# Optimization experiments

Hardware: AMD Instinct MI355X
Metric: run time of the kernel (lower is better)

## Reference

```python
import jax, jax.numpy as jnp
import numpy as np

N_NODES = 50000
N_EDGES = 800000
C = 16          # in = hidden = out channels
FE = 8          # num_edge_features
NUM_GRAPHS = 64


def _nnconv(x, src, dst, edge_attr, w_e, b_e, root, bias):
    # edge MLP -> per-edge weight matrix [E, Cin, Cout]
    cin = x.shape[1]
    W = (edge_attr @ w_e + b_e).reshape(-1, cin, root.shape[1])
    msg = jnp.einsum('ei,eio->eo', x[src], W)            # gather + per-edge matvec
    n = x.shape[0]
    agg = jax.ops.segment_sum(msg, dst, num_segments=n)  # scatter-add
    cnt = jax.ops.segment_sum(jnp.ones((msg.shape[0], 1), x.dtype), dst, num_segments=n)
    agg = agg / jnp.maximum(cnt, 1.0)                    # aggr='mean'
    return x @ root + agg + bias


def setup_inputs() -> dict:
    key = jax.random.key(0)
    ks = jax.random.split(key, 12)
    x = jax.random.normal(ks[0], (N_NODES, C), dtype=jnp.float32)
    edge_index = jax.random.randint(ks[1], (2, N_EDGES), 0, N_NODES, dtype=jnp.int64)
    edge_attr = jax.random.uniform(ks[2], (N_EDGES, FE), dtype=jnp.float32)
    batch = jnp.sort(jax.random.randint(ks[3], (N_NODES,), 0, NUM_GRAPHS, dtype=jnp.int64))
    s = 1.0 / np.sqrt(C)
    se = 1.0 / np.sqrt(FE)
    we1 = jax.random.normal(ks[4], (FE, C * C), dtype=jnp.float32) * se
    be1 = jnp.zeros((C * C,), dtype=jnp.float32)
    root1 = jax.random.normal(ks[5], (C, C), dtype=jnp.float32) * s
    bias1 = jnp.zeros((C,), dtype=jnp.float32)
    we2 = jax.random.normal(ks[6], (FE, C * C), dtype=jnp.float32) * se
    be2 = jnp.zeros((C * C,), dtype=jnp.float32)
    root2 = jax.random.normal(ks[7], (C, C), dtype=jnp.float32) * s
    bias2 = jnp.zeros((C,), dtype=jnp.float32)
    return {"x": x, "edge_index": edge_index, "edge_attr": edge_attr, "batch": batch,
            "we1": we1, "be1": be1, "root1": root1, "bias1": bias1,
            "we2": we2, "be2": be2, "root2": root2, "bias2": bias2}


def reference(x, edge_index, edge_attr, batch,
              we1, be1, root1, bias1, we2, be2, root2, bias2):
    src, dst = edge_index[0], edge_index[1]
    # layer 1 (activation=None -> identity; dropout_prob=0 -> identity)
    h = _nnconv(x, src, dst, edge_attr, we1, be1, root1, bias1)
    # layer 2
    h = _nnconv(h, src, dst, edge_attr, we2, be2, root2, bias2)
    # global mean pool per graph, then flatten
    sums = jax.ops.segment_sum(h, batch, num_segments=NUM_GRAPHS)
    cnts = jax.ops.segment_sum(jnp.ones((h.shape[0], 1), h.dtype), batch, num_segments=NUM_GRAPHS)
    pooled = sums / jnp.maximum(cnts, 1.0)
    return pooled.reshape(-1)
```

## Files before the change

kernel.cpp:

```cpp
#include <hip/hip_runtime.h>

#define NN 50000
#define NE 800000
#define NG 64
#define NB ((NN + 255) / 256)
#define WSTR 164

__global__ __launch_bounds__(256) void histk(const int* __restrict__ dst,
                                             int* __restrict__ deg) {
    int e = blockIdx.x * 256 + threadIdx.x;
    if (e < NE) atomicAdd(&deg[dst[e]], 1);
}

__global__ __launch_bounds__(256) void bsumk(const int* __restrict__ deg,
                                             int* __restrict__ bsum) {
    int idx = blockIdx.x * 256 + threadIdx.x;
    int v = (idx < NN) ? deg[idx] : 0;
#pragma unroll
    for (int off = 32; off > 0; off >>= 1) v += __shfl_down(v, off);
    __shared__ int ws[4];
    int lane = threadIdx.x & 63, w = threadIdx.x >> 6;
    if (lane == 0) ws[w] = v;
    __syncthreads();
    if (threadIdx.x == 0) bsum[blockIdx.x] = ws[0] + ws[1] + ws[2] + ws[3];
}

__global__ __launch_bounds__(256) void bscank(const int* __restrict__ bsum,
                                              int* __restrict__ boffs) {
    int tid = threadIdx.x;
    int v = (tid < NB) ? bsum[tid] : 0;
    int lane = tid & 63, w = tid >> 6;
    int t = v;
#pragma unroll
    for (int off = 1; off < 64; off <<= 1) {
        int u = __shfl_up(t, off);
        if (lane >= off) t += u;
    }
    __shared__ int ws[4];
    if (lane == 63) ws[w] = t;
    __syncthreads();
    int add = 0;
    for (int k = 0; k < w; k++) add += ws[k];
    if (tid < NB) boffs[tid] = add + t - v;
}

__global__ __launch_bounds__(256) void fscank(const int* __restrict__ deg,
                                              const int* __restrict__ boffs,
                                              int* __restrict__ row,
                                              int* __restrict__ cur) {
    int idx = blockIdx.x * 256 + threadIdx.x;
    int v = (idx < NN) ? deg[idx] : 0;
    int lane = threadIdx.x & 63, w = threadIdx.x >> 6;
    int t = v;
#pragma unroll
    for (int off = 1; off < 64; off <<= 1) {
        int u = __shfl_up(t, off);
        if (lane >= off) t += u;
    }
    __shared__ int ws[4];
    if (lane == 63) ws[w] = t;
    __syncthreads();
    int add = boffs[blockIdx.x];
    for (int k = 0; k < w; k++) add += ws[k];
    int ex = add + t - v;
    if (idx < NN) { row[idx] = ex; cur[idx] = ex; }
    else if (idx == NN) row[NN] = ex;
}

__global__ __launch_bounds__(256) void scatk(const int* __restrict__ src,
                                             const int* __restrict__ dst,
                                             const float* __restrict__ ea,
                                             int* __restrict__ cur,
                                             float* __restrict__ rec) {
    int e = blockIdx.x * 256 + threadIdx.x;
    if (e >= NE) return;
    int d = dst[e];
    int pos = atomicAdd(&cur[d], 1);
    float4 a = *(const float4*)(ea + (size_t)e * 8);
    float4 b = *(const float4*)(ea + (size_t)e * 8 + 4);
    float4* r = (float4*)(rec + (size_t)pos * 16);
    float4 r0; r0.x = __int_as_float(src[e]); r0.y = a.x; r0.z = a.y; r0.w = a.z;
    float4 r1; r1.x = a.w; r1.y = b.x; r1.z = b.y; r1.w = b.z;
    float4 r2; r2.x = b.w; r2.y = 0.f; r2.z = 0.f; r2.w = 0.f;
    float4 r3; r3.x = 0.f; r3.y = 0.f; r3.z = 0.f; r3.w = 0.f;
    r[0] = r0; r[1] = r1; r[2] = r2; r[3] = r3;
}

template <bool POOL>
__global__ __launch_bounds__(256) void fusedk(const float* __restrict__ xin,
                                              const int* __restrict__ row,
                                              const float* __restrict__ rec,
                                              const float* __restrict__ we,
                                              const float* __restrict__ be,
                                              const float* __restrict__ root,
                                              const float* __restrict__ bias,
                                              const int* __restrict__ batch,
                                              float* __restrict__ out,
                                              float* __restrict__ gsum,
                                              float* __restrict__ gcnt) {
    __shared__ float wt[16 * WSTR];
    __shared__ float pls[16][WSTR];
    __shared__ float bs[16];
    __shared__ float gacc[16][16];
    __shared__ int gcnta[16];
    int tid = threadIdx.x;
    for (int idx = tid; idx < 2048; idx += 256) {
        int f = idx >> 8; int i = (idx >> 4) & 15; int o = idx & 15;
        wt[o * WSTR + f * 16 + i] = we[idx];
    }
    {
        int i = tid >> 4, o = tid & 15;
        wt[o * WSTR + 128 + i] = be[tid];
        wt[o * WSTR + 144 + i] = root[tid];
    }
    if (tid < 16) bs[tid] = bias[tid];
    if (POOL) {
        gacc[tid >> 4][tid & 15] = 0.f;
        if (tid < 16) gcnta[tid] = 0;
    }

    int g = tid >> 4, t = tid & 15;
    int v = blockIdx.x * 16 + g;
    int r0 = row[v], r1 = row[v + 1];

    float p0 = 0.f, p1 = 0.f, p2 = 0.f, p3 = 0.f;
    float p4 = 0.f, p5 = 0.f, p6 = 0.f, p7 = 0.f, s = 0.f;
    for (int pos = r0; pos < r1; ++pos) {
        const float4* rp = (const float4*)(rec + (size_t)pos * 16);
        float4 c0 = rp[0];
        float4 c1 = rp[1];
        float4 c2 = rp[2];
        int sn = __float_as_int(c0.x);
        float xv = xin[(size_t)sn * 16 + t];
        p0 += c0.y * xv; p1 += c0.z * xv; p2 += c0.w * xv; p3 += c1.x * xv;
        p4 += c1.y * xv; p5 += c1.z * xv; p6 += c1.w * xv; p7 += c2.x * xv;
        s += xv;
    }
    pls[g][0 * 16 + t] = p0; pls[g][1 * 16 + t] = p1;
    pls[g][2 * 16 + t] = p2; pls[g][3 * 16 + t] = p3;
    pls[g][4 * 16 + t] = p4; pls[g][5 * 16 + t] = p5;
    pls[g][6 * 16 + t] = p6; pls[g][7 * 16 + t] = p7;
    pls[g][128 + t] = s;
    pls[g][144 + t] = xin[(size_t)v * 16 + t];
    __syncthreads();

    int o = t;
    const float4* pv = (const float4*)pls[g];
    const float4* wc = (const float4*)(wt + o * WSTR);
    float agg = 0.f;
#pragma unroll
    for (int k = 0; k < 36; k++) {
        float4 a = pv[k]; float4 wv = wc[k];
        agg += a.x * wv.x + a.y * wv.y + a.z * wv.z + a.w * wv.w;
    }
    float r = 0.f;
#pragma unroll
    for (int k = 36; k < 40; k++) {
        float4 a = pv[k]; float4 wv = wc[k];
        r += a.x * wv.x + a.y * wv.y + a.z * wv.z + a.w * wv.w;
    }
    int dg = r1 - r0;
    float h = r + agg / (float)(dg > 1 ? dg : 1) + bs[o];

    if (!POOL) {
        out[(size_t)v * 16 + o] = h;
    } else {
        int bmin = batch[blockIdx.x * 16];
        int b = batch[v];
        int slot = b - bmin;
        if (slot < 16) {
            atomicAdd(&gacc[slot][o], h);
            if (o == 0) atomicAdd(&gcnta[slot], 1);
        } else {
            atomicAdd(&gsum[(size_t)b * 16 + o], h);
            if (o == 0) atomicAdd(&gcnt[b], 1.0f);
        }
        __syncthreads();
        if (gcnta[g] > 0) {
            atomicAdd(&gsum[(size_t)(bmin + g) * 16 + o], gacc[g][o]);
            if (o == 0) atomicAdd(&gcnt[bmin + g], (float)gcnta[g]);
        }
    }
}

__global__ void fink(const float* __restrict__ gsum,
                     const float* __restrict__ gcnt,
                     float* __restrict__ out) {
    int i = blockIdx.x * 256 + threadIdx.x;
    if (i < NG * 16) out[i] = gsum[i] / fmaxf(gcnt[i >> 4], 1.0f);
}

extern "C" void kernel_launch(void* const* d_in, const int* in_sizes, int n_in,
                              void* d_out, int out_size, void* d_ws, size_t ws_size,
                              hipStream_t stream) {
    const float* x     = (const float*)d_in[0];
    const int*   ei    = (const int*)d_in[1];
    const float* ea    = (const float*)d_in[2];
    const int*   batch = (const int*)d_in[3];
    const float* we1   = (const float*)d_in[4];
    const float* be1   = (const float*)d_in[5];
    const float* root1 = (const float*)d_in[6];
    const float* bias1 = (const float*)d_in[7];
    const float* we2   = (const float*)d_in[8];
    const float* be2   = (const float*)d_in[9];
    const float* root2 = (const float*)d_in[10];
    const float* bias2 = (const float*)d_in[11];

    float* ws = (float*)d_ws;
    float* rec  = ws;
    float* h1   = rec + (size_t)NE * 16;
    int*   row  = (int*)(h1 + (size_t)NN * 16);
    int*   cur  = row + NN + 1;
    int*   deg  = cur + NN;
    int*   bsum = deg + NN;
    int*   boffs= bsum + NB;
    float* gsum = (float*)(boffs + NB);
    float* gcnt = gsum + NG * 16;

    hipMemsetAsync(deg, 0, (size_t)(NN + 2 * NB + NG * 16 + NG) * 4, stream);

    const int* src = ei;
    const int* dst = ei + NE;

    int gE = (NE + 255) / 256;
    int gV = NN / 16;

    histk<<<gE, 256, 0, stream>>>(dst, deg);
    bsumk<<<NB, 256, 0, stream>>>(deg, bsum);
    bscank<<<1, 256, 0, stream>>>(bsum, boffs);
    fscank<<<NB, 256, 0, stream>>>(deg, boffs, row, cur);
    scatk<<<gE, 256, 0, stream>>>(src, dst, ea, cur, rec);

    fusedk<false><<<gV, 256, 0, stream>>>(x, row, rec, we1, be1, root1, bias1,
                                          batch, h1, gsum, gcnt);
    fusedk<true><<<gV, 256, 0, stream>>>(h1, row, rec, we2, be2, root2, bias2,
                                         batch, h1 , gsum, gcnt);

    fink<<<4, 256, 0, stream>>>(gsum, gcnt, (float*)d_out);
}
```

Measured before the change: 206.2 us.

## Split edge records into compact attr and src arrays, batch gathers in fused kernel

The per-edge CSR record shrinks from 64 bytes (src plus padded attributes) to 32 bytes of attributes, with source indices moved to a separate int array. The scatter kernel writes both with nontemporal stores. The fused aggregation loop loads 16 source indices cooperatively and broadcasts them with shuffles, and it unrolls the x gathers four at a time to raise memory-level parallelism. The aim is to halve record traffic in both layers and hide gather latency, at the cost of larger code and remainder loops.

```diff
diff --git a/kernel.cpp b/kernel.cpp
--- a/kernel.cpp
+++ b/kernel.cpp
@@ -5,6 +5,8 @@
 #define NG 64
 #define NB ((NN + 255) / 256)
 #define WSTR 164
+
+typedef float nfloat4 __attribute__((ext_vector_type(4)));
 
 __global__ __launch_bounds__(256) void histk(const int* __restrict__ dst,
                                              int* __restrict__ deg) {
@@ -71,25 +73,25 @@
                                              const int* __restrict__ dst,
                                              const float* __restrict__ ea,
                                              int* __restrict__ cur,
-                                             float* __restrict__ rec) {
+                                             float* __restrict__ rec,
+                                             int* __restrict__ srcp) {
     int e = blockIdx.x * 256 + threadIdx.x;
     if (e >= NE) return;
     int d = dst[e];
     int pos = atomicAdd(&cur[d], 1);
-    float4 a = *(const float4*)(ea + (size_t)e * 8);
-    float4 b = *(const float4*)(ea + (size_t)e * 8 + 4);
-    float4* r = (float4*)(rec + (size_t)pos * 16);
-    float4 r0; r0.x = __int_as_float(src[e]); r0.y = a.x; r0.z = a.y; r0.w = a.z;
-    float4 r1; r1.x = a.w; r1.y = b.x; r1.z = b.y; r1.w = b.z;
-    float4 r2; r2.x = b.w; r2.y = 0.f; r2.z = 0.f; r2.w = 0.f;
-    float4 r3; r3.x = 0.f; r3.y = 0.f; r3.z = 0.f; r3.w = 0.f;
-    r[0] = r0; r[1] = r1; r[2] = r2; r[3] = r3;
+    nfloat4 a = *(const nfloat4*)(ea + (size_t)e * 8);
+    nfloat4 b = *(const nfloat4*)(ea + (size_t)e * 8 + 4);
+    nfloat4* r = (nfloat4*)(rec + (size_t)pos * 8);
+    __builtin_nontemporal_store(a, r);
+    __builtin_nontemporal_store(b, r + 1);
+    __builtin_nontemporal_store(src[e], &srcp[pos]);
 }
 
 template <bool POOL>
 __global__ __launch_bounds__(256) void fusedk(const float* __restrict__ xin,
                                               const int* __restrict__ row,
                                               const float* __restrict__ rec,
+                                              const int* __restrict__ srcp,
                                               const float* __restrict__ we,
                                               const float* __restrict__ be,
                                               const float* __restrict__ root,
@@ -120,22 +122,76 @@
     }
 
     int g = tid >> 4, t = tid & 15;
+    int wl = tid & 63;
+    int gl = wl & ~15;
     int v = blockIdx.x * 16 + g;
     int r0 = row[v], r1 = row[v + 1];
 
     float p0 = 0.f, p1 = 0.f, p2 = 0.f, p3 = 0.f;
     float p4 = 0.f, p5 = 0.f, p6 = 0.f, p7 = 0.f, s = 0.f;
-    for (int pos = r0; pos < r1; ++pos) {
-        const float4* rp = (const float4*)(rec + (size_t)pos * 16);
-        float4 c0 = rp[0];
-        float4 c1 = rp[1];
-        float4 c2 = rp[2];
-        int sn = __float_as_int(c0.x);
+
+    int full_end = r0 + ((r1 - r0) & ~15);
+    for (int base = r0; base < full_end; base += 16) {
+        int sv = srcp[base + t];
+#pragma unroll
+        for (int c = 0; c < 16; c += 4) {
+            int s0 = __shfl(sv, gl + c + 0);
+            int s1 = __shfl(sv, gl + c + 1);
+            int s2 = __shfl(sv, gl + c + 2);
+            int s3 = __shfl(sv, gl + c + 3);
+            float x0 = xin[(size_t)s0 * 16 + t];
+            float x1 = xin[(size_t)s1 * 16 + t];
+            float x2 = xin[(size_t)s2 * 16 + t];
+            float x3 = xin[(size_t)s3 * 16 + t];
+            const float4* q0 = (const float4*)(rec + (size_t)(base + c) * 8);
+            float4 a0 = q0[0], b0 = q0[1];
+            float4 a1 = q0[2], b1 = q0[3];
+            float4 a2 = q0[4], b2 = q0[5];
+            float4 a3 = q0[6], b3 = q0[7];
+            p0 += a0.x * x0; p1 += a0.y * x0; p2 += a0.z * x0; p3 += a0.w * x0;
+            p4 += b0.x * x0; p5 += b0.y * x0; p6 += b0.z * x0; p7 += b0.w * x0; s += x0;
+            p0 += a1.x * x1; p1 += a1.y * x1; p2 += a1.z * x1; p3 += a1.w * x1;
+            p4 += b1.x * x1; p5 += b1.y * x1; p6 += b1.z * x1; p7 += b1.w * x1; s += x1;
+            p0 += a2.x * x2; p1 += a2.y * x2; p2 += a2.z * x2; p3 += a2.w * x2;
+            p4 += b2.x * x2; p5 += b2.y * x2; p6 += b2.z * x2; p7 += b2.w * x2; s += x2;
+            p0 += a3.x * x3; p1 += a3.y * x3; p2 += a3.z * x3; p3 += a3.w * x3;
+            p4 += b3.x * x3; p5 += b3.y * x3; p6 += b3.z * x3; p7 += b3.w * x3; s += x3;
+        }
+    }
+    int pos = full_end;
+    int pend = full_end + ((r1 - full_end) & ~3);
+    for (; pos < pend; pos += 4) {
+        int s0 = srcp[pos + 0];
+        int s1 = srcp[pos + 1];
+        int s2 = srcp[pos + 2];
+        int s3 = srcp[pos + 3];
+        float x0 = xin[(size_t)s0 * 16 + t];
+        float x1 = xin[(size_t)s1 * 16 + t];
+        float x2 = xin[(size_t)s2 * 16 + t];
+        float x3 = xin[(size_t)s3 * 16 + t];
+        const float4* q = (const float4*)(rec + (size_t)pos * 8);
+        float4 a0 = q[0], b0 = q[1];
+        float4 a1 = q[2], b1 = q[3];
+        float4 a2 = q[4], b2 = q[5];
+        float4 a3 = q[6], b3 = q[7];
+        p0 += a0.x * x0; p1 += a0.y * x0; p2 += a0.z * x0; p3 += a0.w * x0;
+        p4 += b0.x * x0; p5 += b0.y * x0; p6 += b0.z * x0; p7 += b0.w * x0; s += x0;
+        p0 += a1.x * x1; p1 += a1.y * x1; p2 += a1.z * x1; p3 += a1.w * x1;
+        p4 += b1.x * x1; p5 += b1.y * x1; p6 += b1.z * x1; p7 += b1.w * x1; s += x1;
+        p0 += a2.x * x2; p1 += a2.y * x2; p2 += a2.z * x2; p3 += a2.w * x2;
+        p4 += b2.x * x2; p5 += b2.y * x2; p6 += b2.z * x2; p7 += b2.w * x2; s += x2;
+        p0 += a3.x * x3; p1 += a3.y * x3; p2 += a3.z * x3; p3 += a3.w * x3;
+        p4 += b3.x * x3; p5 += b3.y * x3; p6 += b3.z * x3; p7 += b3.w * x3; s += x3;
+    }
+    for (; pos < r1; ++pos) {
+        int sn = srcp[pos];
         float xv = xin[(size_t)sn * 16 + t];
-        p0 += c0.y * xv; p1 += c0.z * xv; p2 += c0.w * xv; p3 += c1.x * xv;
-        p4 += c1.y * xv; p5 += c1.z * xv; p6 += c1.w * xv; p7 += c2.x * xv;
-        s += xv;
-    }
+        const float4* q = (const float4*)(rec + (size_t)pos * 8);
+        float4 a = q[0], b = q[1];
+        p0 += a.x * xv; p1 += a.y * xv; p2 += a.z * xv; p3 += a.w * xv;
+        p4 += b.x * xv; p5 += b.y * xv; p6 += b.z * xv; p7 += b.w * xv; s += xv;
+    }
+
     pls[g][0 * 16 + t] = p0; pls[g][1 * 16 + t] = p1;
     pls[g][2 * 16 + t] = p2; pls[g][3 * 16 + t] = p3;
     pls[g][4 * 16 + t] = p4; pls[g][5 * 16 + t] = p5;
@@ -208,8 +264,9 @@
 
     float* ws = (float*)d_ws;
     float* rec  = ws;
-    float* h1   = rec + (size_t)NE * 16;
-    int*   row  = (int*)(h1 + (size_t)NN * 16);
+    float* h1   = rec + (size_t)NE * 8;
+    int*   srcp = (int*)(h1 + (size_t)NN * 16);
+    int*   row  = srcp + NE;
     int*   cur  = row + NN + 1;
     int*   deg  = cur + NN;
     int*   bsum = deg + NN;
@@ -229,11 +286,11 @@
     bsumk<<<NB, 256, 0, stream>>>(deg, bsum);
     bscank<<<1, 256, 0, stream>>>(bsum, boffs);
     fscank<<<NB, 256, 0, stream>>>(deg, boffs, row, cur);
-    scatk<<<gE, 256, 0, stream>>>(src, dst, ea, cur, rec);
-
-    fusedk<false><<<gV, 256, 0, stream>>>(x, row, rec, we1, be1, root1, bias1,
+    scatk<<<gE, 256, 0, stream>>>(src, dst, ea, cur, rec, srcp);
+
+    fusedk<false><<<gV, 256, 0, stream>>>(x, row, rec, srcp, we1, be1, root1, bias1,
                                           batch, h1, gsum, gcnt);
-    fusedk<true><<<gV, 256, 0, stream>>>(h1, row, rec, we2, be2, root2, bias2,
+    fusedk<true><<<gV, 256, 0, stream>>>(h1, row, rec, srcp, we2, be2, root2, bias2,
                                          batch, h1 , gsum, gcnt);
 
     fink<<<4, 256, 0, stream>>>(gsum, gcnt, (float*)d_out);
```

Result: slower. 264.3 us (+28.2%).
